# Performance work log

Hardware: AMD Instinct MI355X
Metric: run time of the kernel (lower is better)

The kernel has to match this reference:

```python
import jax, jax.numpy as jnp
import numpy as np

N_QUBITS = 20
BATCH = 16


def setup_inputs() -> dict:
    key = jax.random.key(0)
    k1, k2 = jax.random.split(key)
    phi = jax.random.normal(k1, (BATCH, 2 ** N_QUBITS), dtype=jnp.float32)
    thetas = jax.random.normal(k2, (BATCH, N_QUBITS), dtype=jnp.float32)
    return {"phi": phi, "thetas": thetas}


def reference(phi, thetas):
    """Apply per-qubit RX(theta) rotations to the state vector.

    phi: [B, 2**n] real float32 initial amplitudes (cast to complex64).
    thetas: [B, n] rotation angles, qubit 0 = most-significant bit
    (matches torch view([B] + [2]*n) axis ordering, applied sequentially).
    Returns real/imag stacked: [B, 2**n, 2] float32.
    """
    B, S = phi.shape
    n = N_QUBITS
    c = jnp.cos(thetas / 2).astype(jnp.complex64)          # [B, n]
    s = (-1j * jnp.sin(thetas / 2)).astype(jnp.complex64)  # [B, n]
    state = phi.astype(jnp.complex64)                      # [B, S]
    for i in range(n):  # fixed small loop over qubits (butterfly stages)
        left = 2 ** i
        right = S // (2 * left)
        st = state.reshape(B, left, 2, right)
        a = st[:, :, 0, :]
        b = st[:, :, 1, :]
        ci = c[:, i, None, None]
        si = s[:, i, None, None]
        na = ci * a + si * b
        nb = si * a + ci * b
        state = jnp.stack([na, nb], axis=2).reshape(B, S)
    return jnp.stack([state.real, state.imag], axis=-1)
```

## Files before the change

### kernel.cpp

```cpp
#include <hip/hip_runtime.h>

#define NQ 20

__device__ __forceinline__ float bcast_first(float x) {
    return __int_as_float(__builtin_amdgcn_readfirstlane(__float_as_int(x)));
}

__device__ __forceinline__ void bfly(float C, float SV, float2& a, float2& b) {
    float2 na = make_float2(C * a.x + SV * b.y, C * a.y - SV * b.x);
    float2 nb = make_float2(C * b.x + SV * a.y, C * b.y - SV * a.x);
    a = na; b = nb;
}

__device__ __forceinline__ int swz1(int l) { return l ^ (((l >> 7) & 7) << 2); }

__global__ __launch_bounds__(64) void rx_pass1(
        const float* __restrict__ phi, const float* __restrict__ thetas,
        float2* __restrict__ out) {
    __shared__ float2 lds[2048];
    const int lane = threadIdx.x;
    const int W = blockIdx.x;
    const int b = W >> 9;
    const int base = (W & 511) << 11;
    const float* ph = phi + ((size_t)b << NQ) + base;
    float2* op = out + ((size_t)b << NQ) + base;

    float c[11], sv[11];
#pragma unroll
    for (int beta = 0; beta < 11; ++beta) {
        float th = 0.5f * thetas[b * NQ + (NQ - 1 - beta)];
        c[beta]  = bcast_first(cosf(th));
        sv[beta] = bcast_first(sinf(th));
    }

    float2 v[32];
#pragma unroll
    for (int k4 = 0; k4 < 8; ++k4) {
        float4 t = *(const float4*)(ph + (k4 << 8) + (lane << 2));
        v[k4 * 4 + 0] = make_float2(t.x, 0.f);
        v[k4 * 4 + 1] = make_float2(t.y, 0.f);
        v[k4 * 4 + 2] = make_float2(t.z, 0.f);
        v[k4 * 4 + 3] = make_float2(t.w, 0.f);
    }

    const int regbit1[5]  = {0, 1, 8, 9, 10};
    const int regmask1[5] = {1, 2, 4, 8, 16};
#pragma unroll
    for (int t = 0; t < 5; ++t) {
        const float C = c[regbit1[t]], SV = sv[regbit1[t]];
        const int m = regmask1[t];
#pragma unroll
        for (int r = 0; r < 32; ++r)
            if (!(r & m)) bfly(C, SV, v[r], v[r | m]);
    }

#pragma unroll
    for (int k4 = 0; k4 < 8; ++k4) {
        int low0 = (k4 << 8) + (lane << 2);
        int s0 = swz1(low0);
        *(float4*)&lds[s0]     = make_float4(v[k4*4+0].x, v[k4*4+0].y, v[k4*4+1].x, v[k4*4+1].y);
        *(float4*)&lds[s0 + 2] = make_float4(v[k4*4+2].x, v[k4*4+2].y, v[k4*4+3].x, v[k4*4+3].y);
    }
    __syncthreads();

    {
        const int g = lane >> 2, lam = lane & 3;
        float2 w2[32];
#pragma unroll
        for (int r = 0; r < 32; ++r) {
            int l = (g << 7) | (r << 2) | lam;
            w2[r] = lds[swz1(l)];
        }
#pragma unroll
        for (int t = 0; t < 5; ++t) {
            const float C = c[2 + t], SV = sv[2 + t];
            const int m = 1 << t;
#pragma unroll
            for (int r = 0; r < 32; ++r)
                if (!(r & m)) bfly(C, SV, w2[r], w2[r | m]);
        }
#pragma unroll
        for (int r = 0; r < 32; ++r) {
            int l = (g << 7) | (r << 2) | lam;
            lds[swz1(l)] = w2[r];
        }
    }
    __syncthreads();

    float4 u[16];
#pragma unroll
    for (int m = 0; m < 16; ++m) {
        int l0 = (lane << 1) | ((m & 1) << 7) | (((m >> 1) & 1) << 8)
               | (((m >> 2) & 1) << 9) | (((m >> 3) & 1) << 10);
        u[m] = *(float4*)&lds[swz1(l0)];
    }
    {
        const float C = c[7], SV = sv[7];
#pragma unroll
        for (int m = 0; m < 16; m += 2) {
            float4 A = u[m], B = u[m + 1];
            u[m]     = make_float4(C*A.x + SV*B.y, C*A.y - SV*B.x, C*A.z + SV*B.w, C*A.w - SV*B.z);
            u[m + 1] = make_float4(C*B.x + SV*A.y, C*B.y - SV*A.x, C*B.z + SV*A.w, C*B.w - SV*A.z);
        }
    }
#pragma unroll
    for (int m = 0; m < 16; ++m) {
        int l0 = (lane << 1) | ((m & 1) << 7) | (((m >> 1) & 1) << 8)
               | (((m >> 2) & 1) << 9) | (((m >> 3) & 1) << 10);
        *(float4*)(op + l0) = u[m];
    }
}

__global__ __launch_bounds__(512) void rx_pass2(
        const float* __restrict__ thetas, float2* __restrict__ out) {
    __shared__ float2 buf[8192];
    const int tid = threadIdx.x;
    const int lane = tid & 63;
    const int w = tid >> 6;
    const int b = blockIdx.x >> 7;
    const int lb = blockIdx.x & 127;
    float2* p = out + ((size_t)b << NQ) + (lb << 4);

    float c[9], sv[9];
#pragma unroll
    for (int i = 0; i < 9; ++i) {
        float th = 0.5f * thetas[b * NQ + (8 - i)];
        c[i]  = bcast_first(cosf(th));
        sv[i] = bcast_first(sinf(th));
    }

#pragma unroll
    for (int i = 0; i < 8; ++i) {
        int f = (i << 9) | tid;
        int h = f >> 3, j = f & 7;
        float4 t = *(const float4*)(p + h * 2048 + (j << 1));
        *(float4*)&buf[(h << 4) | (((j << 1) ^ ((h & 7) << 1)))] = t;
    }
    __syncthreads();

    const int l = (w << 1) | (lane >> 5);
    const int g5 = lane & 31;
    float2 v[16];
#pragma unroll
    for (int r = 0; r < 16; ++r) {
        int h = (r << 5) | g5;
        v[r] = buf[(h << 4) | (l ^ ((h & 7) << 1))];
    }

#pragma unroll
    for (int t = 0; t < 5; ++t) {
        const float C = c[t], SV = sv[t];
        const int m = 1 << t;
#pragma unroll
        for (int r = 0; r < 16; ++r) {
            float pr = __shfl_xor(v[r].x, m, 64);
            float pi = __shfl_xor(v[r].y, m, 64);
            v[r] = make_float2(C * v[r].x + SV * pi, C * v[r].y - SV * pr);
        }
    }
#pragma unroll
    for (int t = 0; t < 4; ++t) {
        const float C = c[5 + t], SV = sv[5 + t];
        const int m = 1 << t;
#pragma unroll
        for (int r = 0; r < 16; ++r)
            if (!(r & m)) bfly(C, SV, v[r], v[r | m]);
    }

#pragma unroll
    for (int r = 0; r < 16; ++r) {
        int h = (r << 5) | g5;
        buf[(h << 4) | (l ^ ((h & 7) << 1))] = v[r];
    }
    __syncthreads();

#pragma unroll
    for (int i = 0; i < 8; ++i) {
        int f = (i << 9) | tid;
        int h = f >> 3, j = f & 7;
        float4 t = *(float4*)&buf[(h << 4) | (((j << 1) ^ ((h & 7) << 1)))];
        *(float4*)(p + h * 2048 + (j << 1)) = t;
    }
}

extern "C" void kernel_launch(void* const* d_in, const int* in_sizes, int n_in,
                              void* d_out, int out_size, void* d_ws, size_t ws_size,
                              hipStream_t stream) {
    const float* phi    = (const float*)d_in[0];
    const float* thetas = (const float*)d_in[1];
    float2* out = (float2*)d_out;
    rx_pass1<<<8192, 64, 0, stream>>>(phi, thetas, out);
    rx_pass2<<<2048, 512, 0, stream>>>(thetas, out);
}
```

Measured before the change: 245.0 us.

## Restructure pass2 to in-register butterflies with 256 threads and direct global stores

```diff
diff --git a/kernel.cpp b/kernel.cpp
--- a/kernel.cpp
+++ b/kernel.cpp
@@ -9,6 +9,12 @@
 __device__ __forceinline__ void bfly(float C, float SV, float2& a, float2& b) {
     float2 na = make_float2(C * a.x + SV * b.y, C * a.y - SV * b.x);
     float2 nb = make_float2(C * b.x + SV * a.y, C * b.y - SV * a.x);
+    a = na; b = nb;
+}
+
+__device__ __forceinline__ void bfly4(float C, float SV, float4& a, float4& b) {
+    float4 na = make_float4(C*a.x + SV*b.y, C*a.y - SV*b.x, C*a.z + SV*b.w, C*a.w - SV*b.z);
+    float4 nb = make_float4(C*b.x + SV*a.y, C*b.y - SV*a.x, C*b.z + SV*a.w, C*b.w - SV*a.z);
     a = na; b = nb;
 }
 
@@ -111,12 +117,14 @@
     }
 }
 
-__global__ __launch_bounds__(512) void rx_pass2(
+__device__ __forceinline__ int ppos(int h, int q) {
+    return (h << 4) + (((q ^ (h & 7) ^ ((h >> 5) & 7)) & 7) << 1);
+}
+
+__global__ __launch_bounds__(256) void rx_pass2(
         const float* __restrict__ thetas, float2* __restrict__ out) {
     __shared__ float2 buf[8192];
     const int tid = threadIdx.x;
-    const int lane = tid & 63;
-    const int w = tid >> 6;
     const int b = blockIdx.x >> 7;
     const int lb = blockIdx.x & 127;
     float2* p = out + ((size_t)b << NQ) + (lb << 4);
@@ -130,56 +138,57 @@
     }
 
 #pragma unroll
-    for (int i = 0; i < 8; ++i) {
-        int f = (i << 9) | tid;
+    for (int i = 0; i < 16; ++i) {
+        int f = (i << 8) | tid;
         int h = f >> 3, j = f & 7;
         float4 t = *(const float4*)(p + h * 2048 + (j << 1));
-        *(float4*)&buf[(h << 4) | (((j << 1) ^ ((h & 7) << 1)))] = t;
-    }
-    __syncthreads();
-
-    const int l = (w << 1) | (lane >> 5);
-    const int g5 = lane & 31;
-    float2 v[16];
-#pragma unroll
-    for (int r = 0; r < 16; ++r) {
-        int h = (r << 5) | g5;
-        v[r] = buf[(h << 4) | (l ^ ((h & 7) << 1))];
-    }
-
-#pragma unroll
-    for (int t = 0; t < 5; ++t) {
-        const float C = c[t], SV = sv[t];
-        const int m = 1 << t;
-#pragma unroll
-        for (int r = 0; r < 16; ++r) {
-            float pr = __shfl_xor(v[r].x, m, 64);
-            float pi = __shfl_xor(v[r].y, m, 64);
-            v[r] = make_float2(C * v[r].x + SV * pi, C * v[r].y - SV * pr);
-        }
-    }
-#pragma unroll
-    for (int t = 0; t < 4; ++t) {
-        const float C = c[5 + t], SV = sv[5 + t];
-        const int m = 1 << t;
-#pragma unroll
-        for (int r = 0; r < 16; ++r)
-            if (!(r & m)) bfly(C, SV, v[r], v[r | m]);
-    }
-
-#pragma unroll
-    for (int r = 0; r < 16; ++r) {
-        int h = (r << 5) | g5;
-        buf[(h << 4) | (l ^ ((h & 7) << 1))] = v[r];
-    }
-    __syncthreads();
-
-#pragma unroll
-    for (int i = 0; i < 8; ++i) {
-        int f = (i << 9) | tid;
-        int h = f >> 3, j = f & 7;
-        float4 t = *(float4*)&buf[(h << 4) | (((j << 1) ^ ((h & 7) << 1)))];
-        *(float4*)(p + h * 2048 + (j << 1)) = t;
+        *(float4*)&buf[ppos(h, j)] = t;
+    }
+    __syncthreads();
+
+    {
+        const int hl = tid & 31;
+        const int j  = tid >> 5;
+        float4 w[16];
+#pragma unroll
+        for (int m = 0; m < 16; ++m)
+            w[m] = *(float4*)&buf[ppos((m << 5) | hl, j)];
+#pragma unroll
+        for (int t = 0; t < 4; ++t) {
+            const float C = c[5 + t], SV = sv[5 + t];
+            const int msk = 1 << t;
+#pragma unroll
+            for (int m = 0; m < 16; ++m)
+                if (!(m & msk)) bfly4(C, SV, w[m], w[m | msk]);
+        }
+#pragma unroll
+        for (int m = 0; m < 16; ++m)
+            *(float4*)&buf[ppos((m << 5) | hl, j)] = w[m];
+    }
+    __syncthreads();
+
+    {
+        const int hh = tid >> 4;
+        const int ll = tid & 15;
+        float2 v[32];
+#pragma unroll
+        for (int r = 0; r < 32; ++r) {
+            int h = (hh << 5) | r;
+            v[r] = buf[ppos(h, ll >> 1) + (ll & 1)];
+        }
+#pragma unroll
+        for (int t = 0; t < 5; ++t) {
+            const float C = c[t], SV = sv[t];
+            const int msk = 1 << t;
+#pragma unroll
+            for (int r = 0; r < 32; ++r)
+                if (!(r & msk)) bfly(C, SV, v[r], v[r | msk]);
+        }
+#pragma unroll
+        for (int r = 0; r < 32; ++r) {
+            int h = (hh << 5) | r;
+            p[h * 2048 + ll] = v[r];
+        }
     }
 }
 
@@ -190,5 +199,5 @@
     const float* thetas = (const float*)d_in[1];
     float2* out = (float2*)d_out;
     rx_pass1<<<8192, 64, 0, stream>>>(phi, thetas, out);
-    rx_pass2<<<2048, 512, 0, stream>>>(thetas, out);
-}
+    rx_pass2<<<2048, 256, 0, stream>>>(thetas, out);
+}
```

After: 239.7 us. 1.02x faster.
